# Performance work log

Measured on AMD Instinct MI355X. Metric: run time of the kernel, lower is better.

## Reference

```python
import jax, jax.numpy as jnp
import numpy as np

# config constants (match init_kwargs)
K_MAX = 32
T = 0.1
EPS = 1e-08


def setup_inputs() -> dict:
    key = jax.random.key(0)
    k1, k2, k3 = jax.random.split(key, 3)
    S, d_k, d_A = 8, 128, 1024
    B, N = 256, 100000
    scale = d_A ** (-0.5)
    return {
        "z": jax.random.normal(k1, (B, d_A), dtype=jnp.float32),
        "pool_keys": jax.random.normal(k2, (S, N, d_k), dtype=jnp.float32),
        "W_Q": jax.random.normal(k3, (S, d_k, d_A), dtype=jnp.float32) * scale,
        "aspect_weights": jnp.zeros((S,), dtype=jnp.float32),
        "tau": jnp.asarray(0.0, dtype=jnp.float32),
        "lambda_val": jnp.asarray(10.0, dtype=jnp.float32),
        "is_warmup": jnp.asarray(False),
    }


def reference(z, pool_keys, W_Q, aspect_weights, tau, lambda_val, is_warmup):
    # queries: [B, S, d_k]
    queries = jnp.einsum('ska,ba->bsk', W_Q, z)
    qn = queries / (jnp.linalg.norm(queries, axis=-1, keepdims=True) + EPS)
    kn = pool_keys / (jnp.linalg.norm(pool_keys, axis=-1, keepdims=True) + EPS)
    # per-aspect cosine similarity: [B, S, N]
    sim = jnp.einsum('bsk,snk->bsn', qn, kn)
    w = jax.nn.softmax(aspect_weights, axis=0)  # [S]
    s_i = jnp.einsum('s,bsn->bn', w, sim)       # [B, N]

    def warmup_select(_):
        scores, idx = jax.lax.top_k(s_i, K_MAX)
        alpha = jax.nn.softmax(scores / T, axis=-1)
        return (alpha, idx)

    def gate_select(_):
        g = jax.nn.sigmoid(lambda_val * (s_i - tau))
        raw = g * jnp.exp(s_i / T)
        raw = raw / (raw.sum(axis=-1, keepdims=True) + EPS)
        top_raw, idx = jax.lax.top_k(raw, K_MAX)
        alpha = top_raw / (top_raw.sum(axis=-1, keepdims=True) + EPS)
        return (alpha, idx)

    alphas, indices = jax.lax.cond(is_warmup, warmup_select, gate_select, None)
    return (alphas, indices)
```

## Files before the change

kernel.cpp:

```cpp
#include <hip/hip_runtime.h>
#include <hip/hip_bf16.h>
#include <hip/hip_fp8.h>
#include <math.h>

#define B_      256
#define DA      1024
#define S_      8
#define DK      128
#define NKEYS   100000
#define KMAX    32
#define KTOT    1024
#define BN      128
#define BK      64
#define NBLK    ((NKEYS + BN - 1) / BN)
#define GB      8
#define NA_BLK  (B_ / GB * S_)
#define NK_BLK  ((S_ * NKEYS) / 16)
#define KSCALE  16.0f
#define QSCALE  4.0f

typedef __attribute__((ext_vector_type(8))) short short8;
typedef __attribute__((ext_vector_type(4))) float f32x4;

typedef const __attribute__((address_space(1))) unsigned gu32;
typedef __attribute__((address_space(3))) unsigned lu32;
#define GLOAD_LDS16(g, s) __builtin_amdgcn_global_load_lds((gu32*)(g), (lu32*)(s), 16, 0, 0)

__device__ __forceinline__ float bf16_up(short h) {
    union { unsigned u; float f; } cv;
    cv.u = ((unsigned)(unsigned short)h) << 16;
    return cv.f;
}
__device__ __forceinline__ unsigned char f32_to_e4m3(float x) {
    __hip_fp8_e4m3 h(x);
    return (unsigned char)h.__x;
}

__global__ __launch_bounds__(256) void pass_ak_kernel(
    const float* __restrict__ z, const float* __restrict__ wq,
    const float* __restrict__ keys, const float* __restrict__ aw,
    float* __restrict__ QT, unsigned char* __restrict__ Q8,
    float* __restrict__ F, unsigned char* __restrict__ K8)
{
    __shared__ float zsh[GB][DA];
    __shared__ double part[2];

    if (blockIdx.x < NA_BLK) {
        const int ab = blockIdx.x;
        const int b0 = (ab & (B_ / GB - 1)) * GB;
        const int s  = ab >> 5;
        const int tid = threadIdx.x;
        for (int i = tid; i < GB * DA; i += 256)
            zsh[i >> 10][i & 1023] = z[(size_t)(b0 + (i >> 10)) * DA + (i & 1023)];
        __syncthreads();

        const int k = tid & 127;
        const bool act = tid < 128;
        const float* wrow = wq + (size_t)(s * DK + k) * DA;
        double acc[GB] = {};
        if (act) {
            for (int a = 0; a < DA; a += 32) {
                float4 w[8];
                #pragma unroll
                for (int j = 0; j < 8; ++j)
                    w[j] = *reinterpret_cast<const float4*>(wrow + a + 4 * j);
                #pragma unroll
                for (int j = 0; j < 8; ++j) {
                    const int aa = a + 4 * j;
                    #pragma unroll
                    for (int g = 0; g < GB; ++g) {
                        acc[g] += (double)w[j].x * (double)zsh[g][aa + 0];
                        acc[g] += (double)w[j].y * (double)zsh[g][aa + 1];
                        acc[g] += (double)w[j].z * (double)zsh[g][aa + 2];
                        acc[g] += (double)w[j].w * (double)zsh[g][aa + 3];
                    }
                }
            }
        }
        #pragma unroll
        for (int g = 0; g < GB; ++g) {
            double sq = acc[g] * acc[g];
            #pragma unroll
            for (int off = 32; off > 0; off >>= 1) sq += __shfl_down(sq, off);
            if (act && (tid & 63) == 0) part[tid >> 6] = sq;
            __syncthreads();
            const double ss  = part[0] + part[1];
            const double inv = 1.0 / (sqrt(ss) + 1e-8);
            if (act) {
                const float qv = (float)(acc[g] * inv);
                QT[(size_t)(s * DK + k) * B_ + b0 + g] = qv;
                Q8[(size_t)(b0 + g) * KTOT + s * DK + k] = f32_to_e4m3(qv * QSCALE);
            }
            __syncthreads();
        }
    } else {
        float e[S_];
        float mx = aw[0];
        #pragma unroll
        for (int i = 1; i < S_; ++i) mx = fmaxf(mx, aw[i]);
        float se = 0.f;
        #pragma unroll
        for (int i = 0; i < S_; ++i) { e[i] = expf(aw[i] - mx); se += e[i]; }

        const int g = threadIdx.x >> 4, l = threadIdx.x & 15;
        const long long sn = (long long)(blockIdx.x - NA_BLK) * 16 + g;
        const float* row = keys + (size_t)sn * DK + l * 8;
        const float4 r0 = *reinterpret_cast<const float4*>(row + 0);
        const float4 r1 = *reinterpret_cast<const float4*>(row + 4);
        double sq = (double)r0.x * r0.x + (double)r0.y * r0.y +
                    (double)r0.z * r0.z + (double)r0.w * r0.w +
                    (double)r1.x * r1.x + (double)r1.y * r1.y +
                    (double)r1.z * r1.z + (double)r1.w * r1.w;
        #pragma unroll
        for (int off = 1; off < 16; off <<= 1) sq += __shfl_xor(sq, off);
        const int s = (int)(sn / NKEYS);
        const float w = e[s] / se;
        const float f = (float)((double)w / (sqrt(sq) + 1e-8));
        if (l == 0) F[sn] = f;

        const float fs = f * KSCALE;
        const float vv[8] = {r0.x, r0.y, r0.z, r0.w, r1.x, r1.y, r1.z, r1.w};
        unsigned long long pk = 0ull;
        #pragma unroll
        for (int ee = 0; ee < 8; ++ee)
            pk |= (unsigned long long)f32_to_e4m3(vv[ee] * fs) << (8 * ee);
        *reinterpret_cast<unsigned long long*>(K8 + (size_t)sn * DK + l * 8) = pk;
    }
}

__global__ __launch_bounds__(512) void pass_b_kernel(
    const unsigned char* __restrict__ K8, const unsigned char* __restrict__ Q8,
    __hip_bfloat16* __restrict__ C)
{
    __shared__ __align__(16) char smem[32768];
    const int n0 = blockIdx.x * BN;
    const int tid = threadIdx.x;
    const int w = tid >> 6, l = tid & 63;
    const int ln = l & 15, lk = l >> 4;
    const int wm = w >> 1, wn = w & 1;
    const int lr = l >> 2;
    const int gg = (l & 3) * 2;

    f32x4 acc[4][4];
    #pragma unroll
    for (int i = 0; i < 4; ++i)
        #pragma unroll
        for (int j = 0; j < 4; ++j) acc[i][j] = (f32x4){0.f, 0.f, 0.f, 0.f};

    const char* q8 = (const char*)Q8;
    const char* k8 = (const char*)K8;

    auto stage_b = [&](int t) {
        const int kc   = t * BK;
        const int sidx = kc >> 7;
        const int kl   = kc & (DK - 1);
        const int nr   = w * 16 + lr;
        const size_t gn = (size_t)sidx * NKEYS + (n0 + nr);
        const char* g = k8 + gn * DK + kl + ((gg ^ (nr & 6)) << 3);
        GLOAD_LDS16(g, smem + 16384 + (t & 1) * 8192 + w * 1024);
    };

    stage_b(0);

    for (int t = 0; t < 16; ++t) {
        const int kc = t * BK;
        #pragma unroll
        for (int i = 0; i < 2; ++i) {
            const int j  = w + 8 * i;
            const int bq = j * 16 + lr;
            const char* g = q8 + (size_t)bq * KTOT + kc + ((gg ^ (bq & 6)) << 3);
            GLOAD_LDS16(g, smem + j * 1024);
        }
        stage_b(t + 1);
        asm volatile("s_waitcnt vmcnt(1)" ::: "memory");
        __builtin_amdgcn_sched_barrier(0);
        __builtin_amdgcn_s_barrier();
        __builtin_amdgcn_sched_barrier(0);
        const char* bbase = smem + 16384 + (t & 1) * 8192;
        #pragma unroll
        for (int kw = 0; kw < 2; ++kw) {
            const int slot = kw * 4 + lk;
            long af[4], bf[4];
            #pragma unroll
            for (int mi = 0; mi < 4; ++mi) {
                const int r = wm * 64 + mi * 16 + ln;
                af[mi] = *reinterpret_cast<const long*>(smem + r * 64 + ((slot ^ (r & 6)) << 3));
            }
            #pragma unroll
            for (int nf = 0; nf < 4; ++nf) {
                const int nr = wn * 64 + nf * 16 + ln;
                bf[nf] = *reinterpret_cast<const long*>(bbase + nr * 64 + ((slot ^ (nr & 6)) << 3));
            }
            #pragma unroll
            for (int mi = 0; mi < 4; ++mi)
                #pragma unroll
                for (int nf = 0; nf < 4; ++nf)
                    acc[mi][nf] = __builtin_amdgcn_mfma_f32_16x16x32_fp8_fp8(
                        af[mi], bf[nf], acc[mi][nf], 0, 0, 0);
        }
        __builtin_amdgcn_s_barrier();
    }
    asm volatile("s_waitcnt vmcnt(0)" ::: "memory");

    #pragma unroll
    for (int mi = 0; mi < 4; ++mi) {
        #pragma unroll
        for (int nf = 0; nf < 4; ++nf) {
            const int n = n0 + wn * 64 + nf * 16 + ln;
            if (n < NKEYS) {
                #pragma unroll
                for (int r = 0; r < 4; ++r) {
                    const int bq = wm * 64 + mi * 16 + lk * 4 + r;
                    C[(size_t)bq * NKEYS + n] = __float2bfloat16(acc[mi][nf][r]);
                }
            }
        }
    }
}

#define MAXC 2048
#define NV8 12500
#define NSS (NV8 / 8)
#define CTH 1024

__global__ __launch_bounds__(1024) void pass_c_kernel(
    const __hip_bfloat16* __restrict__ C, const float* __restrict__ keys,
    const float* __restrict__ QT, const float* __restrict__ F,
    const float* __restrict__ tau_p, const float* __restrict__ lam_p,
    const unsigned char* __restrict__ warm_p, float* __restrict__ out)
{
    const int b = blockIdx.x, tid = threadIdx.x;
    __shared__ float redA[16], redB[16];
    __shared__ double cval[MAXC];
    __shared__ int cidx[MAXC];
    __shared__ int cnt;
    __shared__ float sh_stat[2];
    __shared__ double topv[KMAX];
    __shared__ int topi[KMAX];

    const __hip_bfloat16* crow = C + (size_t)b * NKEYS;

    float sm = 0.f, sq = 0.f;
    for (int ii = tid; ii < NSS; ii += CTH) {
        const short8 v8 = *reinterpret_cast<const short8*>(crow + (size_t)ii * 64);
        #pragma unroll
        for (int e = 0; e < 8; ++e) {
            const float v = bf16_up(v8[e]);
            sm += v; sq += v * v;
        }
    }
    #pragma unroll
    for (int off = 32; off > 0; off >>= 1) {
        sm += __shfl_down(sm, off);
        sq += __shfl_down(sq, off);
    }
    if ((tid & 63) == 0) { redA[tid >> 6] = sm; redB[tid >> 6] = sq; }
    __syncthreads();
    if (tid == 0) {
        float S1 = 0.f, S2 = 0.f;
        #pragma unroll
        for (int i = 0; i < 16; ++i) { S1 += redA[i]; S2 += redB[i]; }
        const float nsv = (float)(NSS * 8);
        const float mu = S1 / nsv;
        sh_stat[0] = mu;
        sh_stat[1] = sqrtf(fmaxf(S2 / nsv - mu * mu, 1e-12f));
    }
    __syncthreads();
    const float mu = sh_stat[0], sg = sh_stat[1];

    int m = 0;
    #pragma unroll 1
    for (int attempt = 0; attempt < 4; ++attempt) {
        const float ct = (attempt == 0) ? (mu + 3.0f * sg)
                       : (attempt == 1) ? (mu + 2.5f * sg)
                       : (attempt == 2) ? mu : -1e9f;
        __syncthreads();
        if (tid == 0) cnt = 0;
        __syncthreads();
        for (int i = tid; i < NV8; i += CTH) {
            const short8 v8 = *reinterpret_cast<const short8*>(crow + i * 8);
            #pragma unroll
            for (int e = 0; e < 8; ++e) {
                if (bf16_up(v8[e]) >= ct) {
                    const int p = atomicAdd(&cnt, 1);
                    if (p < MAXC) cidx[p] = i * 8 + e;
                }
            }
        }
        __syncthreads();
        m = min(cnt, MAXC);
        if (m >= KMAX) break;
    }

    const int wave = tid >> 6, lane = tid & 63;
    const int si = lane >> 3, kg = lane & 7;
    for (int c = wave; c < m; c += 16) {
        const int n = cidx[c];
        const float f = F[(size_t)si * NKEYS + n];
        const float* krow = keys + ((size_t)si * NKEYS + n) * DK + kg * 16;
        const float4 k0 = *reinterpret_cast<const float4*>(krow + 0);
        const float4 k1 = *reinterpret_cast<const float4*>(krow + 4);
        const float4 k2 = *reinterpret_cast<const float4*>(krow + 8);
        const float4 k3 = *reinterpret_cast<const float4*>(krow + 12);
        const float kf[16] = {k0.x, k0.y, k0.z, k0.w, k1.x, k1.y, k1.z, k1.w,
                              k2.x, k2.y, k2.z, k2.w, k3.x, k3.y, k3.z, k3.w};
        double acc = 0.0;
        #pragma unroll
        for (int j = 0; j < 16; ++j) {
            const float q = QT[(size_t)(si * DK + kg * 16 + j) * B_ + b];
            acc += (double)q * ((double)kf[j] * (double)f);
        }
        #pragma unroll
        for (int off = 1; off < 64; off <<= 1) acc += __shfl_xor(acc, off);
        if (lane == 0) cval[c] = acc;
    }
    __syncthreads();

    if (tid < 64) {
        for (int r = 0; r < KMAX; ++r) {
            double bv = -1e300; int bi = 0x7fffffff; int bp = -1;
            for (int c = tid; c < m; c += 64) {
                const double v = cval[c]; const int ix = cidx[c];
                if (v > bv || (v == bv && ix < bi)) { bv = v; bi = ix; bp = c; }
            }
            #pragma unroll
            for (int off = 32; off > 0; off >>= 1) {
                const double ov = __shfl_xor(bv, off);
                const int oi = __shfl_xor(bi, off);
                const int op = __shfl_xor(bp, off);
                if (ov > bv || (ov == bv && oi < bi)) { bv = ov; bi = oi; bp = op; }
            }
            if (tid == 0) { topv[r] = bv; topi[r] = bi; if (bp >= 0) cval[bp] = -1e301; }
        }
        if (tid == 0) {
            const float lamv = lam_p[0];
            const float tauv = tau_p[0];
            const bool warm = warm_p[0] != 0;
            float al[KMAX];
            float ssum = 0.f;
            if (warm) {
                const float x0 = (float)topv[0] / 0.1f;
                for (int i = 0; i < KMAX; ++i) {
                    const float e = expf((float)topv[i] / 0.1f - x0);
                    al[i] = e; ssum += e;
                }
            } else {
                for (int i = 0; i < KMAX; ++i) {
                    const float v = (float)topv[i];
                    const float g = 1.0f / (1.0f + expf(-(lamv * (v - tauv))));
                    const float rr = g * expf(v / 0.1f);
                    al[i] = rr; ssum += rr;
                }
            }
            for (int i = 0; i < KMAX; ++i) {
                out[b * KMAX + i] = al[i] / ssum;
                out[B_ * KMAX + b * KMAX + i] = (float)topi[i];
            }
        }
    }
}

extern "C" void kernel_launch(void* const* d_in, const int* in_sizes, int n_in,
                              void* d_out, int out_size, void* d_ws, size_t ws_size,
                              hipStream_t stream) {
    const float* z    = (const float*)d_in[0];
    const float* keys = (const float*)d_in[1];
    const float* wq   = (const float*)d_in[2];
    const float* aw   = (const float*)d_in[3];
    const float* tau  = (const float*)d_in[4];
    const float* lam  = (const float*)d_in[5];
    const unsigned char* warm = (const unsigned char*)d_in[6];
    float* out = (float*)d_out;

    char* ws = (char*)d_ws;
    float* QT           = (float*)ws;
    float* F            = (float*)(ws + (1 << 20));
    unsigned char* Q8   = (unsigned char*)(ws + (8 << 20));
    unsigned char* K8   = (unsigned char*)(ws + (16 << 20));
    __hip_bfloat16* C   = (__hip_bfloat16*)(ws + ((size_t)232 << 20));

    pass_ak_kernel<<<dim3(NA_BLK + NK_BLK), 256, 0, stream>>>(z, wq, keys, aw, QT, Q8, F, K8);
    pass_b_kernel<<<dim3(NBLK), 512, 0, stream>>>(K8, Q8, C);
    pass_c_kernel<<<dim3(B_), 1024, 0, stream>>>(C, keys, QT, F, tau, lam, warm, out);
}
```

Measured before the change: 302.2 us.

## Chunk z staging in LDS and unroll candidate-scan loads in top-k pass

Pass A now stages z through LDS in 256-wide chunks instead of the full 1024-wide row. This cuts shared memory per block by 4x, which should allow more resident blocks, at the cost of extra syncthreads per chunk. In pass C, the statistics loop loads two vectors per iteration and the threshold scan loads four, so more global loads are in flight before the compares. The scan unrolling raises register pressure and code size.

Result: faster. 292.0 us (-3.4%).

```diff
diff --git a/kernel.cpp b/kernel.cpp
--- a/kernel.cpp
+++ b/kernel.cpp
@@ -14,6 +14,7 @@
 #define BK      64
 #define NBLK    ((NKEYS + BN - 1) / BN)
 #define GB      8
+#define ZCH     256
 #define NA_BLK  (B_ / GB * S_)
 #define NK_BLK  ((S_ * NKEYS) / 16)
 #define KSCALE  16.0f
@@ -42,7 +43,7 @@
     float* __restrict__ QT, unsigned char* __restrict__ Q8,
     float* __restrict__ F, unsigned char* __restrict__ K8)
 {
-    __shared__ float zsh[GB][DA];
+    __shared__ float zsh[GB][ZCH];
     __shared__ double part[2];
 
     if (blockIdx.x < NA_BLK) {
@@ -50,29 +51,33 @@
         const int b0 = (ab & (B_ / GB - 1)) * GB;
         const int s  = ab >> 5;
         const int tid = threadIdx.x;
-        for (int i = tid; i < GB * DA; i += 256)
-            zsh[i >> 10][i & 1023] = z[(size_t)(b0 + (i >> 10)) * DA + (i & 1023)];
-        __syncthreads();
-
         const int k = tid & 127;
         const bool act = tid < 128;
         const float* wrow = wq + (size_t)(s * DK + k) * DA;
         double acc[GB] = {};
-        if (act) {
-            for (int a = 0; a < DA; a += 32) {
-                float4 w[8];
-                #pragma unroll
-                for (int j = 0; j < 8; ++j)
-                    w[j] = *reinterpret_cast<const float4*>(wrow + a + 4 * j);
-                #pragma unroll
-                for (int j = 0; j < 8; ++j) {
-                    const int aa = a + 4 * j;
+
+        for (int ch = 0; ch < DA; ch += ZCH) {
+            __syncthreads();
+            for (int i = tid; i < GB * ZCH; i += 256)
+                zsh[i >> 8][i & (ZCH - 1)] =
+                    z[(size_t)(b0 + (i >> 8)) * DA + ch + (i & (ZCH - 1))];
+            __syncthreads();
+            if (act) {
+                for (int a = 0; a < ZCH; a += 32) {
+                    float4 w[8];
                     #pragma unroll
-                    for (int g = 0; g < GB; ++g) {
-                        acc[g] += (double)w[j].x * (double)zsh[g][aa + 0];
-                        acc[g] += (double)w[j].y * (double)zsh[g][aa + 1];
-                        acc[g] += (double)w[j].z * (double)zsh[g][aa + 2];
-                        acc[g] += (double)w[j].w * (double)zsh[g][aa + 3];
+                    for (int j = 0; j < 8; ++j)
+                        w[j] = *reinterpret_cast<const float4*>(wrow + ch + a + 4 * j);
+                    #pragma unroll
+                    for (int j = 0; j < 8; ++j) {
+                        const int aa = a + 4 * j;
+                        #pragma unroll
+                        for (int g = 0; g < GB; ++g) {
+                            acc[g] += (double)w[j].x * (double)zsh[g][aa + 0];
+                            acc[g] += (double)w[j].y * (double)zsh[g][aa + 1];
+                            acc[g] += (double)w[j].z * (double)zsh[g][aa + 2];
+                            acc[g] += (double)w[j].w * (double)zsh[g][aa + 3];
+                        }
                     }
                 }
             }
@@ -241,12 +246,22 @@
     const __hip_bfloat16* crow = C + (size_t)b * NKEYS;
 
     float sm = 0.f, sq = 0.f;
-    for (int ii = tid; ii < NSS; ii += CTH) {
-        const short8 v8 = *reinterpret_cast<const short8*>(crow + (size_t)ii * 64);
+    for (int ii = tid; ii < NSS; ii += 2 * CTH) {
+        const short8 v0 = *reinterpret_cast<const short8*>(crow + (size_t)ii * 64);
+        const bool ok1 = (ii + CTH) < NSS;
+        short8 v1 = v0;
+        if (ok1) v1 = *reinterpret_cast<const short8*>(crow + (size_t)(ii + CTH) * 64);
         #pragma unroll
         for (int e = 0; e < 8; ++e) {
-            const float v = bf16_up(v8[e]);
+            const float v = bf16_up(v0[e]);
             sm += v; sq += v * v;
+        }
+        if (ok1) {
+            #pragma unroll
+            for (int e = 0; e < 8; ++e) {
+                const float v = bf16_up(v1[e]);
+                sm += v; sq += v * v;
+            }
         }
     }
     #pragma unroll
@@ -277,15 +292,45 @@
         __syncthreads();
         if (tid == 0) cnt = 0;
         __syncthreads();
-        for (int i = tid; i < NV8; i += CTH) {
-            const short8 v8 = *reinterpret_cast<const short8*>(crow + i * 8);
-            #pragma unroll
-            for (int e = 0; e < 8; ++e) {
+        int i = tid;
+        for (; i + 3 * CTH < NV8; i += 4 * CTH) {
+            const short8 v0 = *reinterpret_cast<const short8*>(crow + (size_t)(i          ) * 8);
+            const short8 v1 = *reinterpret_cast<const short8*>(crow + (size_t)(i +     CTH) * 8);
+            const short8 v2 = *reinterpret_cast<const short8*>(crow + (size_t)(i + 2 * CTH) * 8);
+            const short8 v3 = *reinterpret_cast<const short8*>(crow + (size_t)(i + 3 * CTH) * 8);
+            #pragma unroll
+            for (int e = 0; e < 8; ++e)
+                if (bf16_up(v0[e]) >= ct) {
+                    const int p = atomicAdd(&cnt, 1);
+                    if (p < MAXC) cidx[p] = i * 8 + e;
+                }
+            #pragma unroll
+            for (int e = 0; e < 8; ++e)
+                if (bf16_up(v1[e]) >= ct) {
+                    const int p = atomicAdd(&cnt, 1);
+                    if (p < MAXC) cidx[p] = (i + CTH) * 8 + e;
+                }
+            #pragma unroll
+            for (int e = 0; e < 8; ++e)
+                if (bf16_up(v2[e]) >= ct) {
+                    const int p = atomicAdd(&cnt, 1);
+                    if (p < MAXC) cidx[p] = (i + 2 * CTH) * 8 + e;
+                }
+            #pragma unroll
+            for (int e = 0; e < 8; ++e)
+                if (bf16_up(v3[e]) >= ct) {
+                    const int p = atomicAdd(&cnt, 1);
+                    if (p < MAXC) cidx[p] = (i + 3 * CTH) * 8 + e;
+                }
+        }
+        for (; i < NV8; i += CTH) {
+            const short8 v8 = *reinterpret_cast<const short8*>(crow + (size_t)i * 8);
+            #pragma unroll
+            for (int e = 0; e < 8; ++e)
                 if (bf16_up(v8[e]) >= ct) {
                     const int p = atomicAdd(&cnt, 1);
                     if (p < MAXC) cidx[p] = i * 8 + e;
                 }
-            }
         }
         __syncthreads();
         m = min(cnt, MAXC);
```
